# Optimization experiments

Measured on AMD Instinct MI355X. Metric: run time of the kernel, lower is better.

The kernel has to match this reference:

```python
import jax, jax.numpy as jnp
import numpy as np

B, T, D, S, EXP = 4, 2048, 1024, 16, 2
E = D * EXP  # expanded channels = 2048


def setup_inputs() -> dict:
    key = jax.random.key(0)
    ks = jax.random.split(key, 8)
    s = 0.02
    f = jnp.float32
    return {
        "x": jax.random.normal(ks[0], (B, T, D), f),
        "in_w": jax.random.normal(ks[1], (2 * E, D), f) * s,
        "in_b": jnp.zeros((2 * E,), f),
        "conv_w": jax.random.normal(ks[2], (E, 1, 3), f) * s,  # depthwise conv, groups=E
        "conv_b": jnp.zeros((E,), f),
        "dt_w": jax.random.normal(ks[3], (E, E), f) * s,
        "dt_b": jnp.zeros((E,), f),
        "B_w": jax.random.normal(ks[4], (S, E), f) * s,
        "B_b": jnp.zeros((S,), f),
        "C_w": jax.random.normal(ks[5], (S, E), f) * s,
        "C_b": jnp.zeros((S,), f),
        "D_w": jax.random.normal(ks[6], (S, E), f) * s,
        "D_b": jnp.zeros((S,), f),
        "out_w": jax.random.normal(ks[7], (D, E), f) * s,
        "out_b": jnp.zeros((D,), f),
    }


def reference(x, in_w, in_b, conv_w, conv_b, dt_w, dt_b, B_w, B_b, C_w, C_b, D_w, D_b, out_w, out_b):
    silu = jax.nn.silu
    # in_proj -> split into main / gate, each [B,T,E]
    xp = x @ in_w.T + in_b
    x_main, x_gate = xp[..., :E], xp[..., E:]
    # depthwise temporal conv (kernel 3, pad 1, groups=E), then SiLU
    xc = jax.lax.conv_general_dilated(
        x_main.transpose(0, 2, 1), conv_w, (1,), [(1, 1)],
        dimension_numbers=("NCH", "OIH", "NCH"), feature_group_count=E)
    xc = silu((xc + conv_b[None, :, None]).transpose(0, 2, 1))  # [B,T,E]
    dt = jax.nn.softplus(xc @ dt_w.T + dt_b)                     # [B,T,E]
    Bt = xc @ B_w.T + B_b                                        # [B,T,S]
    Ct = xc @ C_w.T + C_b
    Dt = xc @ D_w.T + D_b
    decay = jnp.exp(jnp.clip(-dt.mean(-1), -10.0, 10.0))         # [B,T] scalar decay per step
    u = Bt * Dt                                                  # [B,T,S] state input

    def step(state, inp):  # state [B,S]
        d, u_t, c_t = inp
        state = state * d[:, None] + u_t
        return state, (c_t * state).sum(-1)  # y_t [B]

    _, ys = jax.lax.scan(step, jnp.zeros((x.shape[0], S), x.dtype),
                         (decay.T, u.transpose(1, 0, 2), Ct.transpose(1, 0, 2)))
    y = ys.T[..., None] * silu(x_gate)  # broadcast [B,T,1] -> [B,T,E] (matches .expand)
    return x + (y @ out_w.T + out_b)    # dropout in eval mode = identity
```

## Files before the change

kernel.cpp:

```cpp
#include <hip/hip_runtime.h>
#include <hip/hip_bf16.h>

#define Bsz 4
#define Tsz 2048
#define Dsz 1024
#define Ssz 16
#define Esz 2048
#define Mrows (Bsz*Tsz)

typedef __attribute__((ext_vector_type(8))) short short8;
typedef __attribute__((ext_vector_type(4))) float floatx4;
typedef __attribute__((ext_vector_type(8))) int int8v;
typedef __attribute__((ext_vector_type(4))) int int4v;

__device__ __forceinline__ void async_ld16(const void* g, void* l) {
    __builtin_amdgcn_global_load_lds(
        (const __attribute__((address_space(1))) void*)g,
        (__attribute__((address_space(3))) void*)l,
        16, 0, 0);
}

__device__ __forceinline__ float sigmoidf_(float v) { return 1.f / (1.f + expf(-v)); }
__device__ __forceinline__ float bf2f(unsigned short u) {
    union { unsigned u32; float f; } c; c.u32 = (unsigned)u << 16; return c.f;
}
__device__ __forceinline__ int pk_fp8x4(float a, float b, float c, float d) {
    int lo = __builtin_amdgcn_cvt_pk_fp8_f32(a, b, 0, 0);
    int hi = __builtin_amdgcn_cvt_pk_fp8_f32(c, d, 0, 0);
    return (lo & 0xFFFF) | (hi << 16);
}

#define WAIT_VM(N)   (0xF70 | (N))
#define WAIT_LGKM(N) (0xC07F | ((N) << 8))

#define CV_S0 2097152
#define CV_S1 3145728
#define CV_S2 4194304
#define CV_S3 4718592
__global__ void cvt_all(const float4* __restrict__ x,  const float4* __restrict__ iw,
                        const float4* __restrict__ dw, const float4* __restrict__ ow,
                        int* __restrict__ x8, int* __restrict__ iw8,
                        int* __restrict__ dw8, int* __restrict__ ow8) {
    int i = blockIdx.x * blockDim.x + threadIdx.x;
    const int stride = gridDim.x * blockDim.x;
    for (; i < CV_S3; i += stride) {
        if (i < CV_S0) {
            float4 v = x[i];
            x8[i] = pk_fp8x4(v.x, v.y, v.z, v.w);
        } else if (i < CV_S1) {
            const int j = i - CV_S0;
            float4 v = iw[j];
            iw8[j] = pk_fp8x4(v.x * 64.f, v.y * 64.f, v.z * 64.f, v.w * 64.f);
        } else if (i < CV_S2) {
            const int j = i - CV_S1;
            float4 v = dw[j];
            dw8[j] = pk_fp8x4(v.x * 64.f, v.y * 64.f, v.z * 64.f, v.w * 64.f);
        } else {
            const int j = i - CV_S2;
            float4 v = ow[j];
            ow8[j] = pk_fp8x4(v.x * 64.f, v.y * 64.f, v.z * 64.f, v.w * 64.f);
        }
    }
}

template<int MODE, int SA, int SB>
__launch_bounds__(256, 2)
__global__ void gemm_f8(const unsigned char* __restrict__ A,
                        const unsigned char* __restrict__ Bw,
                        const float* __restrict__ bias,
                        int M, int N, int K,
                        __hip_bfloat16* __restrict__ outb,
                        float* __restrict__ rowsum,
                        const float* __restrict__ resid,
                        const float* __restrict__ ysv,
                        float* __restrict__ outf) {
    __shared__ __align__(16) unsigned char sA[2 * 16384];
    __shared__ __align__(16) unsigned char sB[2 * 16384];

    const int tid  = threadIdx.x;
    const int wave = tid >> 6, lane = tid & 63;
    const int wm = wave >> 1, wn = wave & 1;
    const int q = lane >> 4, lr = lane & 15;

    const int gx = gridDim.x, gy = gridDim.y;
    const int flat = blockIdx.y * gx + blockIdx.x;
    const int stripe = gy >> 3;
    const int xcd = flat & 7, local = flat >> 3;
    const int mt = xcd * stripe + (local % stripe);
    const int nt = local / stripe;
    const int m0 = mt * 128, n0 = nt * 128;

    floatx4 acc[4][4];
#pragma unroll
    for (int i = 0; i < 4; ++i)
#pragma unroll
        for (int j = 0; j < 4; ++j) acc[i][j] = (floatx4){0.f, 0.f, 0.f, 0.f};

    const unsigned char* pa[4];
    const unsigned char* pb[4];
#pragma unroll
    for (int i = 0; i < 4; ++i) {
        const int idx = i * 256 + tid, row = idx >> 3, s = idx & 7;
        pa[i] = A + (size_t)(m0 + row) * K + ((s ^ (row & 7)) * 16);
        pb[i] = Bw + (size_t)(n0 + row) * K + ((s ^ (row & 7)) * 16);
    }

    const int rA = wm * 64 + lr, rB = wn * 64 + lr;
    const int oA0 = rA * 128 + (((2 * q)     ^ (rA & 7)) * 16);
    const int oA1 = rA * 128 + (((2 * q + 1) ^ (rA & 7)) * 16);
    const int oB0 = rB * 128 + (((2 * q)     ^ (rB & 7)) * 16);
    const int oB1 = rB * 128 + (((2 * q + 1) ^ (rB & 7)) * 16);

#define F8_ISSUE(ST) do {                                                      \
        _Pragma("unroll")                                                      \
        for (int i = 0; i < 4; ++i) {                                          \
            async_ld16(pa[i], &sA[(ST) * 16384 + (i * 256 + wave * 64) * 16]); \
            pa[i] += 128;                                                      \
        }                                                                      \
        _Pragma("unroll")                                                      \
        for (int i = 0; i < 4; ++i) {                                          \
            async_ld16(pb[i], &sB[(ST) * 16384 + (i * 256 + wave * 64) * 16]); \
            pb[i] += 128;                                                      \
        }                                                                      \
    } while (0)

#define F8_STEP(ST) do {                                                       \
        asm volatile("" ::: "memory");                                         \
        __builtin_amdgcn_s_waitcnt(WAIT_VM(8));          \
        __builtin_amdgcn_s_barrier();                                          \
        asm volatile("" ::: "memory");                                         \
        int8v a8[4], b8[4];                                                    \
        _Pragma("unroll")                                                      \
        for (int i = 0; i < 4; ++i) {                                          \
            int4v lo = *(const int4v*)&sA[(ST) * 16384 + oA0 + i * 2048];      \
            int4v hi = *(const int4v*)&sA[(ST) * 16384 + oA1 + i * 2048];      \
            a8[i] = __builtin_shufflevector(lo, hi, 0, 1, 2, 3, 4, 5, 6, 7);   \
        }                                                                      \
        _Pragma("unroll")                                                      \
        for (int j = 0; j < 4; ++j) {                                          \
            int4v lo = *(const int4v*)&sB[(ST) * 16384 + oB0 + j * 2048];      \
            int4v hi = *(const int4v*)&sB[(ST) * 16384 + oB1 + j * 2048];      \
            b8[j] = __builtin_shufflevector(lo, hi, 0, 1, 2, 3, 4, 5, 6, 7);   \
        }                                                                      \
        asm volatile("" ::: "memory");                                         \
        __builtin_amdgcn_s_waitcnt(WAIT_LGKM(0));            \
        __builtin_amdgcn_s_barrier();                      \
        asm volatile("" ::: "memory");                                         \
        F8_ISSUE(ST);                               \
        _Pragma("unroll")                                                      \
        for (int i = 0; i < 4; ++i)                                            \
            _Pragma("unroll")                                                  \
            for (int j = 0; j < 4; ++j)                                        \
                acc[i][j] = __builtin_amdgcn_mfma_scale_f32_16x16x128_f8f6f4(  \
                    a8[i], b8[j], acc[i][j], 0, 0, 0, SA, 0, SB);              \
    } while (0)

    const int nit = K >> 8;
    F8_ISSUE(0);
    F8_ISSUE(1);
    for (int it = 0; it < nit; ++it) {
        F8_STEP(0);
        F8_STEP(1);
    }
#undef F8_STEP
#undef F8_ISSUE
    asm volatile("" ::: "memory");
    __builtin_amdgcn_s_waitcnt(WAIT_VM(0));

    if (MODE == 0) {
#pragma unroll
        for (int i = 0; i < 4; ++i) {
            const int row = m0 + wm * 64 + i * 16 + q * 4;
#pragma unroll
            for (int j = 0; j < 4; ++j) {
                const int col = n0 + wn * 64 + j * 16 + lr;
                const float bc = bias[col];
#pragma unroll
                for (int r = 0; r < 4; ++r)
                    outb[(size_t)(row + r) * N + col] = __float2bfloat16(acc[i][j][r] + bc);
            }
        }
    } else if (MODE == 1) {
#pragma unroll
        for (int i = 0; i < 4; ++i) {
            float rs[4] = {0.f, 0.f, 0.f, 0.f};
#pragma unroll
            for (int j = 0; j < 4; ++j) {
                const int col = n0 + wn * 64 + j * 16 + lr;
                const float bc = bias[col];
#pragma unroll
                for (int r = 0; r < 4; ++r) {
                    float v = acc[i][j][r] + bc;
                    float sp = (v > 20.f) ? v : log1pf(expf(v));
                    rs[r] += sp;
                }
            }
#pragma unroll
            for (int r = 0; r < 4; ++r) {
                float v = rs[r];
                v += __shfl_xor(v, 1); v += __shfl_xor(v, 2);
                v += __shfl_xor(v, 4); v += __shfl_xor(v, 8);
                if (lr == 0)
                    atomicAdd(&rowsum[m0 + wm * 64 + i * 16 + q * 4 + r], v);
            }
        }
    } else {
#pragma unroll
        for (int i = 0; i < 4; ++i) {
            const int row = m0 + wm * 64 + i * 16 + q * 4;
#pragma unroll
            for (int j = 0; j < 4; ++j) {
                const int col = n0 + wn * 64 + j * 16 + lr;
                const float bc = bias[col];
#pragma unroll
                for (int r = 0; r < 4; ++r) {
                    const size_t idx = (size_t)(row + r) * N + col;
                    outf[idx] = resid[idx] + ysv[row + r] * acc[i][j][r] + bc;
                }
            }
        }
    }
}

__global__ void conv_gate_k(const __hip_bfloat16* __restrict__ xp,
                            const float* __restrict__ cw,
                            const float* __restrict__ cb,
                            __hip_bfloat16* __restrict__ xc,
                            int2* __restrict__ xc8,
                            int2* __restrict__ s8) {
    const int idx8 = blockIdx.x * blockDim.x + threadIdx.x;
    const int e = (idx8 & (Esz / 8 - 1)) * 8;
    const int r = idx8 >> 8;
    const int t = r & (Tsz - 1);
    const unsigned short* row0 = (const unsigned short*)(xp + (size_t)r * (2 * Esz) + e);
    short8 vm1 = (t > 0)       ? *(const short8*)(row0 - 2 * Esz) : (short8){0,0,0,0,0,0,0,0};
    short8 v00 = *(const short8*)row0;
    short8 vp1 = (t < Tsz - 1) ? *(const short8*)(row0 + 2 * Esz) : (short8){0,0,0,0,0,0,0,0};
    short8 o;
    float sil[8];
#pragma unroll
    for (int k = 0; k < 8; ++k) {
        const int ek = e + k;
        float v = bf2f((unsigned short)vm1[k]) * cw[ek * 3 + 0]
                + bf2f((unsigned short)v00[k]) * cw[ek * 3 + 1]
                + bf2f((unsigned short)vp1[k]) * cw[ek * 3 + 2] + cb[ek];
        sil[k] = v * sigmoidf_(v);
        __hip_bfloat16 h = __float2bfloat16(sil[k]);
        o[k] = *(short*)&h;
    }
    *(short8*)(xc + (size_t)idx8 * 8) = o;
    int2 p;
    p.x = pk_fp8x4(sil[0] * 16.f, sil[1] * 16.f, sil[2] * 16.f, sil[3] * 16.f);
    p.y = pk_fp8x4(sil[4] * 16.f, sil[5] * 16.f, sil[6] * 16.f, sil[7] * 16.f);
    xc8[idx8] = p;

    short8 g = *(const short8*)(row0 + Esz);
    float sg[8];
#pragma unroll
    for (int k = 0; k < 8; ++k) {
        const float gv = bf2f((unsigned short)g[k]);
        sg[k] = gv * sigmoidf_(gv);
    }
    int2 ps;
    ps.x = pk_fp8x4(sg[0] * 16.f, sg[1] * 16.f, sg[2] * 16.f, sg[3] * 16.f);
    ps.y = pk_fp8x4(sg[4] * 16.f, sg[5] * 16.f, sg[6] * 16.f, sg[7] * 16.f);
    s8[idx8] = ps;
}

__global__ void pack_bcd(const float* __restrict__ Bw, const float* __restrict__ Cw,
                         const float* __restrict__ Dw, __hip_bfloat16* __restrict__ Wb) {
    const int idx = blockIdx.x * blockDim.x + threadIdx.x;
    if (idx >= 48 * Esz) return;
    const int row = idx >> 11, col = idx & (Esz - 1);
    float v;
    if (row < 16)      v = Bw[row * Esz + col];
    else if (row < 32) v = Cw[(row - 16) * Esz + col];
    else               v = Dw[(row - 32) * Esz + col];
    Wb[idx] = __float2bfloat16(v);
}

__launch_bounds__(256)
__global__ void bcd_mfma(const __hip_bfloat16* __restrict__ xc,
                         const __hip_bfloat16* __restrict__ Wb,
                         const float* __restrict__ Bb, const float* __restrict__ Cb,
                         const float* __restrict__ Db,
                         float* __restrict__ u, float* __restrict__ Ct) {
    __shared__ __align__(16) __hip_bfloat16 sA[64 * 32];
    __shared__ __align__(16) __hip_bfloat16 sW[48 * 32];
    const int tid = threadIdx.x;
    const int wave = tid >> 6, lane = tid & 63;
    const int q = lane >> 4, lr = lane & 15;
    const int m0 = blockIdx.x * 64;

    floatx4 acc[3];
#pragma unroll
    for (int j = 0; j < 3; ++j) acc[j] = (floatx4){0.f, 0.f, 0.f, 0.f};

    const int ra = wave * 16 + (lane >> 2);
    const int ca = (lane & 3) * 8;

    for (int kt = 0; kt < (Esz >> 5); ++kt) {
        const int k0 = kt << 5;
        __syncthreads();
        async_ld16(&xc[(size_t)(m0 + ra) * Esz + k0 + ca], &sA[wave * 512]);
        if (wave < 3)
            async_ld16(&Wb[(size_t)ra * Esz + k0 + ca], &sW[wave * 512]);
        __syncthreads();

        short8 af = *(const short8*)&sA[(wave * 16 + lr) * 32 + q * 8];
#pragma unroll
        for (int j = 0; j < 3; ++j) {
            short8 wf = *(const short8*)&sW[(j * 16 + lr) * 32 + q * 8];
            acc[j] = __builtin_amdgcn_mfma_f32_16x16x32_bf16(af, wf, acc[j], 0, 0, 0);
        }
    }

    const int row = m0 + wave * 16 + q * 4;
    const float bb = Bb[lr], cbv = Cb[lr], db = Db[lr];
#pragma unroll
    for (int r = 0; r < 4; ++r) {
        const float bt = acc[0][r] + bb;
        const float ct = acc[1][r] + cbv;
        const float dt = acc[2][r] + db;
        u [(size_t)(row + r) * Ssz + lr] = bt * dt;
        Ct[(size_t)(row + r) * Ssz + lr] = ct;
    }
}

__global__ void scan_k(const float* __restrict__ rowsum, const float* __restrict__ u,
                       const float* __restrict__ Ct, float* __restrict__ ys) {
    const int b = blockIdx.x;
    const int tid = threadIdx.x;
    const int lane = tid & 63, wave = tid >> 6;
    __shared__ __align__(16) float su[256 * Ssz];
    __shared__ __align__(16) float sc[256 * Ssz];
    __shared__ float sp[256 * 17];
    __shared__ float sd[256];
    float st = 0.f;
    for (int t0 = 0; t0 < Tsz; t0 += 256) {
        __syncthreads();
        const float4* ub = (const float4*)(u  + ((size_t)b * Tsz + t0) * Ssz);
        const float4* cb = (const float4*)(Ct + ((size_t)b * Tsz + t0) * Ssz);
#pragma unroll
        for (int i = 0; i < 4; ++i) {
            ((float4*)su)[tid + i * 256] = ub[tid + i * 256];
            ((float4*)sc)[tid + i * 256] = cb[tid + i * 256];
        }
        {
            const float m = rowsum[b * Tsz + t0 + tid] * (1.f / (float)Esz);
            sd[tid] = expf(fminf(fmaxf(-m, -10.f), 10.f));
        }
        __syncthreads();
        if (wave == 0 && lane < 16) {
#pragma unroll 8
            for (int i = 0; i < 256; ++i) {
                st = st * sd[i] + su[i * Ssz + lane];
                sp[i * 17 + lane] = sc[i * Ssz + lane] * st;
            }
        }
        __syncthreads();
        float s = 0.f;
#pragma unroll
        for (int j = 0; j < 16; ++j) s += sp[tid * 17 + j];
        ys[b * Tsz + t0 + tid] = s;
    }
}

extern "C" void kernel_launch(void* const* d_in, const int* in_sizes, int n_in,
                              void* d_out, int out_size, void* d_ws, size_t ws_size,
                              hipStream_t stream) {
    const float* x      = (const float*)d_in[0];
    const float* in_w   = (const float*)d_in[1];
    const float* in_b   = (const float*)d_in[2];
    const float* conv_w = (const float*)d_in[3];
    const float* conv_b = (const float*)d_in[4];
    const float* dt_w   = (const float*)d_in[5];
    const float* dt_b   = (const float*)d_in[6];
    const float* B_w    = (const float*)d_in[7];
    const float* B_b    = (const float*)d_in[8];
    const float* C_w    = (const float*)d_in[9];
    const float* C_b    = (const float*)d_in[10];
    const float* D_w    = (const float*)d_in[11];
    const float* D_b    = (const float*)d_in[12];
    const float* out_w  = (const float*)d_in[13];
    const float* out_b  = (const float*)d_in[14];
    float* out = (float*)d_out;

    char* ws = (char*)d_ws;
    auto alloc = [&](size_t bytes) {
        char* p = ws;
        ws += (bytes + 255) & ~(size_t)255;
        return p;
    };
    unsigned char* x_f8    = (unsigned char*)alloc((size_t)Mrows * Dsz);
    unsigned char* inw_f8  = (unsigned char*)alloc((size_t)2 * Esz * Dsz);
    unsigned char* dtw_f8  = (unsigned char*)alloc((size_t)Esz * Esz);
    unsigned char* outw_f8 = (unsigned char*)alloc((size_t)Dsz * Esz);
    __hip_bfloat16* xp_bf  = (__hip_bfloat16*)alloc((size_t)Mrows * 2 * Esz * 2);
    __hip_bfloat16* xc_bf  = (__hip_bfloat16*)alloc((size_t)Mrows * Esz * 2);
    unsigned char* xc_f8   = (unsigned char*)alloc((size_t)Mrows * Esz);
    unsigned char* s_f8    = (unsigned char*)alloc((size_t)Mrows * Esz);
    __hip_bfloat16* wb_bf  = (__hip_bfloat16*)alloc((size_t)48 * Esz * 2);
    float* rowsum = (float*)alloc(Mrows * 4);
    float* u_buf  = (float*)alloc((size_t)Mrows * Ssz * 4);
    float* ct_buf = (float*)alloc((size_t)Mrows * Ssz * 4);
    float* ys_buf = (float*)alloc(Mrows * 4);
    (void)alloc(65536);

    hipMemsetAsync(rowsum, 0, Mrows * 4, stream);

    cvt_all<<<4608, 256, 0, stream>>>((const float4*)x, (const float4*)in_w,
                                      (const float4*)dt_w, (const float4*)out_w,
                                      (int*)x_f8, (int*)inw_f8, (int*)dtw_f8,
                                      (int*)outw_f8);
    pack_bcd<<<48 * Esz / 256, 256, 0, stream>>>(B_w, C_w, D_w, wb_bf);

    gemm_f8<0, 127, 121><<<dim3(4096 / 128, Mrows / 128), 256, 0, stream>>>(
        x_f8, inw_f8, in_b, Mrows, 4096, 1024, xp_bf, nullptr, nullptr, nullptr, nullptr);

    conv_gate_k<<<(Mrows * Esz / 8) / 256, 256, 0, stream>>>(
        xp_bf, conv_w, conv_b, xc_bf, (int2*)xc_f8, (int2*)s_f8);

    gemm_f8<1, 123, 121><<<dim3(Esz / 128, Mrows / 128), 256, 0, stream>>>(
        xc_f8, dtw_f8, dt_b, Mrows, Esz, Esz, nullptr, rowsum, nullptr, nullptr, nullptr);

    bcd_mfma<<<Mrows / 64, 256, 0, stream>>>(xc_bf, wb_bf, B_b, C_b, D_b, u_buf, ct_buf);

    scan_k<<<Bsz, 256, 0, stream>>>(rowsum, u_buf, ct_buf, ys_buf);

    gemm_f8<2, 123, 121><<<dim3(Dsz / 128, Mrows / 128), 256, 0, stream>>>(
        s_f8, outw_f8, out_b, Mrows, Dsz, Esz, nullptr, nullptr, x, ys_buf, out);
}
```

Measured before the change: 418.7 us.

## Simplify FP8 GEMM main loop to single-barrier double buffering

Replaces the two-stage unrolled FP8 MFMA K-loop with a plain loop over 128-wide K tiles. The old loop kept two tiles of async global-to-LDS loads in flight and used two barriers per step; the new one waits for all outstanding loads, syncs once, issues the next tile into the other buffer, then reads LDS and runs the MFMAs. This drops one barrier and an LDS wait per tile, but shortens the prefetch distance to one tile, which leaves less global-load latency hidden. The last iteration also issues a load one tile past the end of K.

```diff
diff --git a/kernel.cpp b/kernel.cpp
--- a/kernel.cpp
+++ b/kernel.cpp
@@ -31,7 +31,6 @@
 }
 
 #define WAIT_VM(N)   (0xF70 | (N))
-#define WAIT_LGKM(N) (0xC07F | ((N) << 8))
 
 #define CV_S0 2097152
 #define CV_S1 3145728
@@ -124,47 +123,35 @@
         }                                                                      \
     } while (0)
 
-#define F8_STEP(ST) do {                                                       \
-        asm volatile("" ::: "memory");                                         \
-        __builtin_amdgcn_s_waitcnt(WAIT_VM(8));          \
-        __builtin_amdgcn_s_barrier();                                          \
-        asm volatile("" ::: "memory");                                         \
-        int8v a8[4], b8[4];                                                    \
-        _Pragma("unroll")                                                      \
-        for (int i = 0; i < 4; ++i) {                                          \
-            int4v lo = *(const int4v*)&sA[(ST) * 16384 + oA0 + i * 2048];      \
-            int4v hi = *(const int4v*)&sA[(ST) * 16384 + oA1 + i * 2048];      \
-            a8[i] = __builtin_shufflevector(lo, hi, 0, 1, 2, 3, 4, 5, 6, 7);   \
-        }                                                                      \
-        _Pragma("unroll")                                                      \
-        for (int j = 0; j < 4; ++j) {                                          \
-            int4v lo = *(const int4v*)&sB[(ST) * 16384 + oB0 + j * 2048];      \
-            int4v hi = *(const int4v*)&sB[(ST) * 16384 + oB1 + j * 2048];      \
-            b8[j] = __builtin_shufflevector(lo, hi, 0, 1, 2, 3, 4, 5, 6, 7);   \
-        }                                                                      \
-        asm volatile("" ::: "memory");                                         \
-        __builtin_amdgcn_s_waitcnt(WAIT_LGKM(0));            \
-        __builtin_amdgcn_s_barrier();                      \
-        asm volatile("" ::: "memory");                                         \
-        F8_ISSUE(ST);                               \
-        _Pragma("unroll")                                                      \
-        for (int i = 0; i < 4; ++i)                                            \
-            _Pragma("unroll")                                                  \
-            for (int j = 0; j < 4; ++j)                                        \
-                acc[i][j] = __builtin_amdgcn_mfma_scale_f32_16x16x128_f8f6f4(  \
-                    a8[i], b8[j], acc[i][j], 0, 0, 0, SA, 0, SB);              \
-    } while (0)
-
-    const int nit = K >> 8;
+    const int ntiles = K >> 7;
     F8_ISSUE(0);
-    F8_ISSUE(1);
-    for (int it = 0; it < nit; ++it) {
-        F8_STEP(0);
-        F8_STEP(1);
-    }
-#undef F8_STEP
+    for (int kt = 0; kt < ntiles; ++kt) {
+        const int st = kt & 1;
+        __builtin_amdgcn_s_waitcnt(WAIT_VM(0));
+        __syncthreads();
+        F8_ISSUE(st ^ 1);
+
+        int8v a8[4], b8[4];
+#pragma unroll
+        for (int i = 0; i < 4; ++i) {
+            int4v lo = *(const int4v*)&sA[st * 16384 + oA0 + i * 2048];
+            int4v hi = *(const int4v*)&sA[st * 16384 + oA1 + i * 2048];
+            a8[i] = __builtin_shufflevector(lo, hi, 0, 1, 2, 3, 4, 5, 6, 7);
+        }
+#pragma unroll
+        for (int j = 0; j < 4; ++j) {
+            int4v lo = *(const int4v*)&sB[st * 16384 + oB0 + j * 2048];
+            int4v hi = *(const int4v*)&sB[st * 16384 + oB1 + j * 2048];
+            b8[j] = __builtin_shufflevector(lo, hi, 0, 1, 2, 3, 4, 5, 6, 7);
+        }
+#pragma unroll
+        for (int i = 0; i < 4; ++i)
+#pragma unroll
+            for (int j = 0; j < 4; ++j)
+                acc[i][j] = __builtin_amdgcn_mfma_scale_f32_16x16x128_f8f6f4(
+                    a8[i], b8[j], acc[i][j], 0, 0, 0, SA, 0, SB);
+    }
 #undef F8_ISSUE
-    asm volatile("" ::: "memory");
     __builtin_amdgcn_s_waitcnt(WAIT_VM(0));
 
     if (MODE == 0) {
```

New measurement: 442.3 us. 1.06x slower.

## Parallelize the scan across time chunks and restructure the B/C/D projection kernel

Applied to the files above, without the earlier changes.

The sequential scan ran in only 4 blocks, one per batch, each walking all 2048 steps serially. It is replaced by a three-phase chunked scan. Phase one runs 32 blocks that each scan a 256-step chunk locally and record the cumulative decay products. Phase two is a tiny carry propagation across chunks. Phase three adds the carried-in state contribution to each output step. The B/C/D projection kernel now uses 32-row tiles with 128 threads, stages a 256-wide K slab of weights in LDS, and loads activations straight from global memory into registers. The costs are two extra kernel launches and fp32 reassociation differences from the chunked decay products.

```diff
diff --git a/kernel.cpp b/kernel.cpp
--- a/kernel.cpp
+++ b/kernel.cpp
@@ -279,39 +279,48 @@
     Wb[idx] = __float2bfloat16(v);
 }
 
-__launch_bounds__(256)
-__global__ void bcd_mfma(const __hip_bfloat16* __restrict__ xc,
-                         const __hip_bfloat16* __restrict__ Wb,
-                         const float* __restrict__ Bb, const float* __restrict__ Cb,
-                         const float* __restrict__ Db,
-                         float* __restrict__ u, float* __restrict__ Ct) {
-    __shared__ __align__(16) __hip_bfloat16 sA[64 * 32];
-    __shared__ __align__(16) __hip_bfloat16 sW[48 * 32];
+__launch_bounds__(128)
+__global__ void bcd_mfma2(const __hip_bfloat16* __restrict__ xc,
+                          const __hip_bfloat16* __restrict__ Wb,
+                          const float* __restrict__ Bb, const float* __restrict__ Cb,
+                          const float* __restrict__ Db,
+                          float* __restrict__ u, float* __restrict__ Ct) {
+    __shared__ __align__(16) __hip_bfloat16 sW[48 * 256];
     const int tid = threadIdx.x;
     const int wave = tid >> 6, lane = tid & 63;
     const int q = lane >> 4, lr = lane & 15;
-    const int m0 = blockIdx.x * 64;
+    const int m0 = blockIdx.x * 32;
 
     floatx4 acc[3];
 #pragma unroll
     for (int j = 0; j < 3; ++j) acc[j] = (floatx4){0.f, 0.f, 0.f, 0.f};
 
-    const int ra = wave * 16 + (lane >> 2);
-    const int ca = (lane & 3) * 8;
-
-    for (int kt = 0; kt < (Esz >> 5); ++kt) {
-        const int k0 = kt << 5;
+    const __hip_bfloat16* arow = xc + (size_t)(m0 + wave * 16 + lr) * Esz;
+
+    for (int kt = 0; kt < 8; ++kt) {
+        const int k0 = kt << 8;
         __syncthreads();
-        async_ld16(&xc[(size_t)(m0 + ra) * Esz + k0 + ca], &sA[wave * 512]);
-        if (wave < 3)
-            async_ld16(&Wb[(size_t)ra * Esz + k0 + ca], &sW[wave * 512]);
+#pragma unroll
+        for (int j = 0; j < 12; ++j) {
+            const int idx = j * 128 + tid;
+            const int row = idx >> 5, ch = idx & 31;
+            async_ld16(&Wb[(size_t)row * Esz + k0 + ch * 8],
+                       (__hip_bfloat16*)sW + idx * 8);
+        }
+        __builtin_amdgcn_s_waitcnt(WAIT_VM(0));
         __syncthreads();
 
-        short8 af = *(const short8*)&sA[(wave * 16 + lr) * 32 + q * 8];
-#pragma unroll
-        for (int j = 0; j < 3; ++j) {
-            short8 wf = *(const short8*)&sW[(j * 16 + lr) * 32 + q * 8];
-            acc[j] = __builtin_amdgcn_mfma_f32_16x16x32_bf16(af, wf, acc[j], 0, 0, 0);
+        short8 af[8];
+#pragma unroll
+        for (int ks = 0; ks < 8; ++ks)
+            af[ks] = *(const short8*)&arow[k0 + ks * 32 + q * 8];
+#pragma unroll
+        for (int ks = 0; ks < 8; ++ks) {
+#pragma unroll
+            for (int j = 0; j < 3; ++j) {
+                short8 wf = *(const short8*)&sW[(j * 16 + lr) * 256 + ks * 32 + q * 8];
+                acc[j] = __builtin_amdgcn_mfma_f32_16x16x32_bf16(af[ks], wf, acc[j], 0, 0, 0);
+            }
         }
     }
 
@@ -327,43 +336,85 @@
     }
 }
 
-__global__ void scan_k(const float* __restrict__ rowsum, const float* __restrict__ u,
-                       const float* __restrict__ Ct, float* __restrict__ ys) {
-    const int b = blockIdx.x;
+__global__ void scanA(const float* __restrict__ rowsum, const float* __restrict__ u,
+                      const float* __restrict__ Ct,
+                      float* __restrict__ ysl, float* __restrict__ pt,
+                      float* __restrict__ send) {
+    const int cid = blockIdx.x;
+    const int b = cid >> 3, c = cid & 7;
+    const int t0 = c * 256;
     const int tid = threadIdx.x;
     const int lane = tid & 63, wave = tid >> 6;
     __shared__ __align__(16) float su[256 * Ssz];
     __shared__ __align__(16) float sc[256 * Ssz];
     __shared__ float sp[256 * 17];
     __shared__ float sd[256];
-    float st = 0.f;
-    for (int t0 = 0; t0 < Tsz; t0 += 256) {
-        __syncthreads();
-        const float4* ub = (const float4*)(u  + ((size_t)b * Tsz + t0) * Ssz);
-        const float4* cb = (const float4*)(Ct + ((size_t)b * Tsz + t0) * Ssz);
-#pragma unroll
-        for (int i = 0; i < 4; ++i) {
-            ((float4*)su)[tid + i * 256] = ub[tid + i * 256];
-            ((float4*)sc)[tid + i * 256] = cb[tid + i * 256];
-        }
-        {
-            const float m = rowsum[b * Tsz + t0 + tid] * (1.f / (float)Esz);
-            sd[tid] = expf(fminf(fmaxf(-m, -10.f), 10.f));
-        }
-        __syncthreads();
-        if (wave == 0 && lane < 16) {
+
+    const float4* ub = (const float4*)(u  + ((size_t)b * Tsz + t0) * Ssz);
+    const float4* cb = (const float4*)(Ct + ((size_t)b * Tsz + t0) * Ssz);
+#pragma unroll
+    for (int i = 0; i < 4; ++i) {
+        ((float4*)su)[tid + i * 256] = ub[tid + i * 256];
+        ((float4*)sc)[tid + i * 256] = cb[tid + i * 256];
+    }
+    {
+        const float m = rowsum[b * Tsz + t0 + tid] * (1.f / (float)Esz);
+        sd[tid] = expf(fminf(fmaxf(-m, -10.f), 10.f));
+    }
+    __syncthreads();
+    if (wave == 0 && lane < 16) {
+        float st = 0.f, P = 1.f;
 #pragma unroll 8
-            for (int i = 0; i < 256; ++i) {
-                st = st * sd[i] + su[i * Ssz + lane];
-                sp[i * 17 + lane] = sc[i * Ssz + lane] * st;
-            }
-        }
-        __syncthreads();
-        float s = 0.f;
-#pragma unroll
-        for (int j = 0; j < 16; ++j) s += sp[tid * 17 + j];
-        ys[b * Tsz + t0 + tid] = s;
-    }
+        for (int i = 0; i < 256; ++i) {
+            const float d = sd[i];
+            st = st * d + su[i * Ssz + lane];
+            sp[i * 17 + lane] = sc[i * Ssz + lane] * st;
+            if (lane == 0) { P *= d; sp[i * 17 + 16] = P; }
+        }
+        send[cid * Ssz + lane] = st;
+    }
+    __syncthreads();
+    float s = 0.f;
+#pragma unroll
+    for (int j = 0; j < 16; ++j) s += sp[tid * 17 + j];
+    ysl[b * Tsz + t0 + tid] = s;
+    pt [b * Tsz + t0 + tid] = sp[tid * 17 + 16];
+}
+
+__global__ void scanB(const float* __restrict__ send, const float* __restrict__ pt,
+                      float* __restrict__ sstart) {
+    const int tid = threadIdx.x;
+    if (tid >= 64) return;
+    const int b = tid >> 4, j = tid & 15;
+    float s = 0.f;
+    for (int c = 0; c < 8; ++c) {
+        const int cid = b * 8 + c;
+        sstart[cid * Ssz + j] = s;
+        const float Pc = pt[b * Tsz + c * 256 + 255];
+        s = send[cid * Ssz + j] + Pc * s;
+    }
+}
+
+__global__ void scanC(const float* __restrict__ ysl, const float* __restrict__ pt,
+                      const float* __restrict__ sstart, const float* __restrict__ Ct,
+                      float* __restrict__ ys) {
+    const int cid = blockIdx.x;
+    const int b = cid >> 3, c = cid & 7;
+    const int t0 = c * 256;
+    const int tid = threadIdx.x;
+    __shared__ float s0[Ssz];
+    if (tid < 16) s0[tid] = sstart[cid * Ssz + tid];
+    __syncthreads();
+    const int g = b * Tsz + t0 + tid;
+    const float4* cr = (const float4*)(Ct + (size_t)g * Ssz);
+    float dot = 0.f;
+#pragma unroll
+    for (int i = 0; i < 4; ++i) {
+        float4 v = cr[i];
+        dot += v.x * s0[i * 4 + 0] + v.y * s0[i * 4 + 1]
+             + v.z * s0[i * 4 + 2] + v.w * s0[i * 4 + 3];
+    }
+    ys[g] = ysl[g] + pt[g] * dot;
 }
 
 extern "C" void kernel_launch(void* const* d_in, const int* in_sizes, int n_in,
@@ -405,6 +456,10 @@
     float* u_buf  = (float*)alloc((size_t)Mrows * Ssz * 4);
     float* ct_buf = (float*)alloc((size_t)Mrows * Ssz * 4);
     float* ys_buf = (float*)alloc(Mrows * 4);
+    float* ysl_buf = (float*)alloc(Mrows * 4);
+    float* pt_buf  = (float*)alloc(Mrows * 4);
+    float* send_buf = (float*)alloc(32 * Ssz * 4);
+    float* sstart_buf = (float*)alloc(32 * Ssz * 4);
     (void)alloc(65536);
 
     hipMemsetAsync(rowsum, 0, Mrows * 4, stream);
@@ -424,9 +479,11 @@
     gemm_f8<1, 123, 121><<<dim3(Esz / 128, Mrows / 128), 256, 0, stream>>>(
         xc_f8, dtw_f8, dt_b, Mrows, Esz, Esz, nullptr, rowsum, nullptr, nullptr, nullptr);
 
-    bcd_mfma<<<Mrows / 64, 256, 0, stream>>>(xc_bf, wb_bf, B_b, C_b, D_b, u_buf, ct_buf);
-
-    scan_k<<<Bsz, 256, 0, stream>>>(rowsum, u_buf, ct_buf, ys_buf);
+    bcd_mfma2<<<Mrows / 32, 128, 0, stream>>>(xc_bf, wb_bf, B_b, C_b, D_b, u_buf, ct_buf);
+
+    scanA<<<32, 256, 0, stream>>>(rowsum, u_buf, ct_buf, ysl_buf, pt_buf, send_buf);
+    scanB<<<1, 64, 0, stream>>>(send_buf, pt_buf, sstart_buf);
+    scanC<<<32, 256, 0, stream>>>(ysl_buf, pt_buf, sstart_buf, ct_buf, ys_buf);
 
     gemm_f8<2, 123, 121><<<dim3(Dsz / 128, Mrows / 128), 256, 0, stream>>>(
         s_f8, outw_f8, out_b, Mrows, Dsz, Esz, nullptr, nullptr, x, ys_buf, out);
```

Result: faster. 385.7 us (-7.9%).
